# Kernel tuning notes

Measured on AMD Instinct MI355X. Metric: run time of the kernel, lower is better.

## Reference

```python
import jax, jax.numpy as jnp
import numpy as np

N, E = 50000, 200000
SIZES = [16, 32, 16]
EDIM = 8
EPS = 1e-5


def setup_inputs() -> dict:
    key = jax.random.key(0)
    ks = jax.random.split(key, 16)
    inp = {
        "x": jax.random.normal(ks[0], (N, SIZES[0]), jnp.float32),
        "edge_attr": jax.random.normal(ks[1], (E, EDIM), jnp.float32),
        "edge_index": jax.random.randint(ks[2], (2, E), 0, N, dtype=jnp.int32),
    }
    ki = 3
    for l in range(2):
        fin, fout = SIZES[l], SIZES[l + 1]
        m = fin * fout
        # xavier-ish init matching torch.nn.init.xavier_uniform_ scales
        inp[f"W1_{l}"] = jax.random.normal(ks[ki], (EDIM, m), jnp.float32) / np.float32(np.sqrt(EDIM)); ki += 1
        inp[f"b1_{l}"] = jnp.zeros((m,), jnp.float32)
        inp[f"W2_{l}"] = jax.random.normal(ks[ki], (m, m), jnp.float32) * np.float32(0.01 / np.sqrt(m)); ki += 1
        inp[f"b2_{l}"] = jnp.zeros((m,), jnp.float32)
        inp[f"root_{l}"] = jax.random.normal(ks[ki], (fin, fout), jnp.float32) / np.float32(np.sqrt(fin)); ki += 1
        inp[f"bias_{l}"] = jnp.zeros((fout,), jnp.float32)
        inp[f"gamma_{l}"] = jnp.ones((fout,), jnp.float32)
        inp[f"beta_{l}"] = jnp.zeros((fout,), jnp.float32)
    return inp


def _lrelu(v):
    return jnp.where(v >= 0, v, 0.01 * v)


def _nnconv(x, src, dst, edge_attr, W1, b1, W2, b2, root, bias, fin, fout):
    # edge MLP -> per-edge weight matrix [E, fin, fout]
    h = _lrelu(edge_attr @ W1 + b1) @ W2 + b2
    h = h.reshape(-1, fin, fout)
    # gather source node features, tiny per-edge matmul
    msg = jnp.einsum('ei,eio->eo', x[src], h)  # [E, fout]
    # scatter-mean aggregate at destination nodes
    agg = jax.ops.segment_sum(msg, dst, num_segments=N)
    deg = jax.ops.segment_sum(jnp.ones((msg.shape[0],), msg.dtype), dst, num_segments=N)
    agg = agg / jnp.maximum(deg, 1.0)[:, None]
    return agg + x @ root + bias


def _bn(v, gamma, beta):
    # BatchNorm1d (training mode: batch stats, biased variance)
    mu = v.mean(0)
    var = v.var(0)
    return (v - mu) * jax.lax.rsqrt(var + EPS) * gamma + beta


def reference(x, edge_attr,
              W1_0, b1_0, W2_0, b2_0, root_0, bias_0, gamma_0, beta_0,
              W1_1, b1_1, W2_1, b2_1, root_1, bias_1, gamma_1, beta_1,
              edge_index):
    src, dst = edge_index[0], edge_index[1]
    h = _nnconv(x, src, dst, edge_attr, W1_0, b1_0, W2_0, b2_0, root_0, bias_0, SIZES[0], SIZES[1])
    h = _lrelu(_bn(h, gamma_0, beta_0))
    h = _nnconv(h, src, dst, edge_attr, W1_1, b1_1, W2_1, b2_1, root_1, bias_1, SIZES[1], SIZES[2])
    return _bn(h, gamma_1, beta_1)
```

## Files before the change

### kernel.cpp

```cpp
#include <hip/hip_runtime.h>
#include <hip/hip_bf16.h>

typedef __attribute__((ext_vector_type(4))) float f32x4;
typedef __attribute__((ext_vector_type(8))) short s16x8;
typedef __attribute__((ext_vector_type(4))) int int4v;

#define DEVI __device__ __forceinline__

constexpr int NN = 50000;
constexpr int NE = 200000;
constexpr float BN_EPS = 1e-5f;

DEVI float bfbits2f(unsigned v) { union { unsigned u; float f; } t; t.u = v << 16; return t.f; }
DEVI float lrelu_f(float v) { return v >= 0.f ? v : 0.01f * v; }

__global__ void k_transpose_w2(const float* __restrict__ A0, const float* __restrict__ A1,
                               __hip_bfloat16* __restrict__ T0, __hip_bfloat16* __restrict__ T1) {
  const float* W2 = blockIdx.y ? A1 : A0;
  __hip_bfloat16* W2T = blockIdx.y ? T1 : T0;
  __shared__ float tile[32][33];
  int bx = blockIdx.x % 16, by = blockIdx.x / 16;
  int t = threadIdx.x;
  int r = t / 32, c = t % 32;
  for (int rr = r; rr < 32; rr += 8)
    tile[rr][c] = W2[(size_t)(by * 32 + rr) * 512 + bx * 32 + c];
  __syncthreads();
  for (int rr = r; rr < 32; rr += 8)
    W2T[(size_t)(bx * 32 + rr) * 512 + by * 32 + c] = __float2bfloat16(tile[c][rr]);
}

__global__ void k_transpose_w1(const float* __restrict__ A0, const float* __restrict__ A1,
                               __hip_bfloat16* __restrict__ T0, __hip_bfloat16* __restrict__ T1) {
  const float* W1 = blockIdx.y ? A1 : A0;
  __hip_bfloat16* W1T = blockIdx.y ? T1 : T0;
  int tid = blockIdx.x * 256 + threadIdx.x;
  if (tid < 8 * 512) {
    int k = tid / 512, n = tid % 512;
    W1T[n * 8 + k] = __float2bfloat16(W1[tid]);
  }
}

__global__ void k_count(const int* __restrict__ dst, int* __restrict__ cnt) {
  int e = blockIdx.x * 256 + threadIdx.x;
  if (e < NE) atomicAdd(&cnt[dst[e]], 1);
}

constexpr int SCAN_ELEMS = 1024;
__global__ void k_scan1(const int* __restrict__ cnt, int* __restrict__ base, int* __restrict__ aux, int n) {
  __shared__ int sw[256];
  int b = blockIdx.x, t = threadIdx.x;
  int i0 = b * SCAN_ELEMS + t * 4;
  int v[4]; int s = 0;
  #pragma unroll
  for (int j = 0; j < 4; j++) { int idx = i0 + j; v[j] = (idx < n) ? cnt[idx] : 0; s += v[j]; }
  sw[t] = s; __syncthreads();
  for (int d = 1; d < 256; d <<= 1) {
    int val = (t >= d) ? sw[t - d] : 0;
    __syncthreads();
    sw[t] += val;
    __syncthreads();
  }
  int run = (t > 0) ? sw[t - 1] : 0;
  #pragma unroll
  for (int j = 0; j < 4; j++) { int idx = i0 + j; if (idx < n) base[idx] = run; run += v[j]; }
  if (t == 255) aux[b] = sw[255];
}

__global__ void k_scan2(int* aux, int nb) {
  if (threadIdx.x == 0 && blockIdx.x == 0) {
    int run = 0;
    for (int i = 0; i < nb; i++) { int v = aux[i]; aux[i] = run; run += v; }
  }
}

__global__ void k_scan3(int* __restrict__ base, int* __restrict__ cursor, const int* __restrict__ aux, int n) {
  int i = blockIdx.x * 256 + threadIdx.x;
  if (i < n) { int v = base[i] + aux[i / SCAN_ELEMS]; base[i] = v; cursor[i] = v; }
}

__global__ void k_place(const int* __restrict__ dst, int* __restrict__ cursor, int* __restrict__ perm) {
  int e = blockIdx.x * 256 + threadIdx.x;
  if (e < NE) { int p = atomicAdd(&cursor[dst[e]], 1); perm[p] = e; }
}

template <int FIN, int FOUT>
__global__ __launch_bounds__(512, 2)
void k_edge(const float* __restrict__ x, const float* __restrict__ ea,
            const int* __restrict__ srcI,
            const __hip_bfloat16* __restrict__ W1T, const float* __restrict__ b1,
            const __hip_bfloat16* __restrict__ W2T, const float* __restrict__ b2,
            __hip_bfloat16* __restrict__ msgb)
{
  static_assert(FOUT == 32 || FOUT == 16, "");
  constexpr int TM = 512;
  constexpr int CG = 32;
  constexpr int NCGI = 16;
  constexpr int KH = 256;
  constexpr int NKC = 4;
  constexpr int NOT = FOUT / 16;
  constexpr int BSTRIDE = KH * 2 + 16;
  constexpr int XLDS = TM + 8;

  __shared__ __align__(16) char ubuf[65536];
  __shared__ __align__(16) __hip_bfloat16 eab[TM][8];
  __shared__ __align__(16) __hip_bfloat16 xlt[FIN][XLDS];

  const int tid = threadIdx.x;
  const int lane = tid & 63, w = tid >> 6;
  const int l15 = lane & 15, l4 = lane >> 4;
  const int e0 = blockIdx.x * TM;
  const int rem = min(TM, NE - e0);
  const int wrow0 = w * 64;

  {
    int er = e0 + min(tid, rem - 1);
    float4 v0 = *(const float4*)(ea + (size_t)er * 8);
    float4 v1 = *(const float4*)(ea + (size_t)er * 8 + 4);
    __hip_bfloat16* p = &eab[tid][0];
    p[0] = __float2bfloat16(v0.x); p[1] = __float2bfloat16(v0.y);
    p[2] = __float2bfloat16(v0.z); p[3] = __float2bfloat16(v0.w);
    p[4] = __float2bfloat16(v1.x); p[5] = __float2bfloat16(v1.y);
    p[6] = __float2bfloat16(v1.z); p[7] = __float2bfloat16(v1.w);
    int s = srcI[er];
    #pragma unroll
    for (int q = 0; q < FIN / 4; q++) {
      float4 xv4 = *(const float4*)(x + (size_t)s * FIN + q * 4);
      xlt[q * 4 + 0][tid] = __float2bfloat16(xv4.x);
      xlt[q * 4 + 1][tid] = __float2bfloat16(xv4.y);
      xlt[q * 4 + 2][tid] = __float2bfloat16(xv4.z);
      xlt[q * 4 + 3][tid] = __float2bfloat16(xv4.w);
    }
  }
  __syncthreads();

  f32x4 msg[4][NOT];
  #pragma unroll
  for (int rt = 0; rt < 4; rt++)
    #pragma unroll
    for (int ot = 0; ot < NOT; ot++) msg[rt][ot] = (f32x4)(0.f);

  s16x8 af[NKC][4][2];
  int4v sr0, sr1;

  for (int sw = 0; sw < 2; ++sw) {
    {
      int n = tid >> 4, s0 = tid & 15;
      const char* gp = (const char*)(W2T + (size_t)n * 512 + sw * KH);
      sr0 = *(const int4v*)(gp + s0 * 16);
      sr1 = *(const int4v*)(gp + (s0 + 16) * 16);
    }
    s16x8 afe[4];
    #pragma unroll
    for (int rt = 0; rt < 4; rt++) {
      s16x8 tv = *(const s16x8*)(&eab[wrow0 + rt * 16 + l15][0]);
      afe[rt] = (lane < 16) ? tv : (s16x8)0;
    }
    char* gme = ubuf + w * 8192;
    #pragma unroll
    for (int kc = 0; kc < NKC; kc++) {
      #pragma unroll
      for (int ct = 0; ct < 4; ct++) {
        int c = sw * KH + kc * 64 + ct * 16 + l15;
        s16x8 bw = *(const s16x8*)(W1T + c * 8);
        bw = (lane < 16) ? bw : (s16x8)0;
        float b1v = b1[c];
        #pragma unroll
        for (int rt = 0; rt < 4; rt++) {
          f32x4 d = __builtin_amdgcn_mfma_f32_16x16x32_bf16(afe[rt], bw, (f32x4)(0.f), 0, 0, 0);
          #pragma unroll
          for (int r = 0; r < 4; r++) {
            int rloc = rt * 16 + l4 * 4 + r;
            float gv = d[r] + b1v;
            gv = gv >= 0.f ? gv : 0.01f * gv;
            int byt = (rloc * 128 + (ct * 16 + l15) * 2) ^ (((rloc + (rloc >> 2)) & 3) << 5);
            *(__hip_bfloat16*)(gme + byt) = __float2bfloat16(gv);
          }
        }
      }
      #pragma unroll
      for (int rt = 0; rt < 4; rt++)
        #pragma unroll
        for (int ks = 0; ks < 2; ks++) {
          int rloc = rt * 16 + l15;
          int byt = (rloc * 128 + (ks * 32 + l4 * 8) * 2) ^ (((rloc + (rloc >> 2)) & 3) << 5);
          af[kc][rt][ks] = *(const s16x8*)(gme + byt);
        }
    }
    #pragma unroll
    for (int kc = 0; kc < NKC; kc++)
      #pragma unroll
      for (int rt = 0; rt < 4; rt++)
        #pragma unroll
        for (int ks = 0; ks < 2; ks++)
          asm volatile("" : "+v"(af[kc][rt][ks]));
    __syncthreads();
    {
      int n = tid >> 4, s0 = tid & 15;
      char* bb = ubuf;
      *(int4v*)(bb + n * BSTRIDE + s0 * 16) = sr0;
      *(int4v*)(bb + n * BSTRIDE + (s0 + 16) * 16) = sr1;
    }
    __syncthreads();

    for (int cgi = 0; cgi < NCGI; ++cgi) {
      if (cgi + 1 < NCGI) {
        int n = tid >> 4, s0 = tid & 15;
        const char* gp = (const char*)(W2T + (size_t)((cgi + 1) * CG + n) * 512 + sw * KH);
        sr0 = *(const int4v*)(gp + s0 * 16);
        sr1 = *(const int4v*)(gp + (s0 + 16) * 16);
      }
      const char* bb = ubuf + (cgi & 1) * (CG * BSTRIDE);
      f32x4 acc[4][2];
      #pragma unroll
      for (int rt = 0; rt < 4; rt++) { acc[rt][0] = (f32x4)(0.f); acc[rt][1] = (f32x4)(0.f); }

      #pragma unroll
      for (int kc = 0; kc < NKC; kc++)
        #pragma unroll
        for (int ct = 0; ct < 2; ct++) {
          int c = ct * 16 + l15;
          #pragma unroll
          for (int ks = 0; ks < 2; ks++) {
            const s16x8 bw = *(const s16x8*)(bb + c * BSTRIDE + kc * 128 + ks * 64 + l4 * 16);
            #pragma unroll
            for (int rt = 0; rt < 4; rt++)
              acc[rt][ct] = __builtin_amdgcn_mfma_f32_16x16x32_bf16(af[kc][rt][ks], bw, acc[rt][ct], 0, 0, 0);
          }
        }

      #pragma unroll
      for (int ct = 0; ct < 2; ct++) {
        float b2v = (sw == 0) ? b2[cgi * CG + ct * 16 + l15] : 0.f;
        const int iv = (FOUT == 32) ? cgi : (cgi * 2 + ct);
        const int ot = (FOUT == 32) ? ct : 0;
        #pragma unroll
        for (int rt = 0; rt < 4; rt++) {
          int rbase = wrow0 + rt * 16 + l4 * 4;
          ushort4 xv = *(const ushort4*)(&xlt[iv][rbase]);
          msg[rt][ot][0] += bfbits2f(xv.x) * (acc[rt][ct][0] + b2v);
          msg[rt][ot][1] += bfbits2f(xv.y) * (acc[rt][ct][1] + b2v);
          msg[rt][ot][2] += bfbits2f(xv.z) * (acc[rt][ct][2] + b2v);
          msg[rt][ot][3] += bfbits2f(xv.w) * (acc[rt][ct][3] + b2v);
        }
      }
      if (cgi + 1 < NCGI) {
        int n = tid >> 4, s0 = tid & 15;
        char* bw2 = ubuf + ((cgi + 1) & 1) * (CG * BSTRIDE);
        *(int4v*)(bw2 + n * BSTRIDE + s0 * 16) = sr0;
        *(int4v*)(bw2 + n * BSTRIDE + (s0 + 16) * 16) = sr1;
      }
      __syncthreads();
    }
  }

  #pragma unroll
  for (int rt = 0; rt < 4; rt++)
    #pragma unroll
    for (int r = 0; r < 4; r++) {
      int row = wrow0 + rt * 16 + l4 * 4 + r;
      if (row < rem) {
        #pragma unroll
        for (int ot = 0; ot < NOT; ot++)
          msgb[(size_t)(e0 + row) * FOUT + ot * 16 + l15] = __float2bfloat16(msg[rt][ot][r]);
      }
    }
}

template <int FIN, int FOUT>
__global__ void k_node_agg(const __hip_bfloat16* __restrict__ msgb, const int* __restrict__ perm,
                           const int* __restrict__ base,
                           const float* __restrict__ x,
                           const float* __restrict__ root,
                           const float* __restrict__ bias,
                           float* __restrict__ h)
{
  __shared__ float rl[FIN * FOUT];
  constexpr int NPB = 256 / FOUT;
  int t = threadIdx.x;
  for (int i = t; i < FIN * FOUT; i += 256) rl[i] = root[i];
  __syncthreads();
  int n = blockIdx.x * NPB + t / FOUT;
  int o = t % FOUT;
  if (n >= NN) return;
  int s = base[n];
  int e = (n + 1 < NN) ? base[n + 1] : NE;
  float sum = 0.f;
  for (int j = s; j < e; j++)
    sum += __bfloat162float(msgb[(size_t)perm[j] * FOUT + o]);
  float acc = sum / fmaxf((float)(e - s), 1.f) + bias[o];
  #pragma unroll
  for (int i = 0; i < FIN; i++)
    acc += x[(size_t)n * FIN + i] * rl[i * FOUT + o];
  h[(size_t)n * FOUT + o] = acc;
}

template <int FOUT>
__global__ void k_stats(const float* __restrict__ h, float* __restrict__ ssum, float* __restrict__ ssq) {
  constexpr int RPB = 256 / FOUT;
  int t = threadIdx.x;
  int o = t % FOUT, rr = t / FOUT;
  float v = 0.f, v2 = 0.f;
  for (int r = blockIdx.x * RPB + rr; r < NN; r += gridDim.x * RPB) {
    float y = h[(size_t)r * FOUT + o];
    v += y; v2 += y * y;
  }
  #pragma unroll
  for (int d = FOUT; d < 64; d <<= 1) { v += __shfl_xor(v, d); v2 += __shfl_xor(v2, d); }
  __shared__ float sv[4][32], sq[4][32];
  int wv = t >> 6, ln = t & 63;
  if (ln < FOUT) { sv[wv][ln] = v; sq[wv][ln] = v2; }
  __syncthreads();
  if (t < FOUT) {
    float a = 0.f, b = 0.f;
    #pragma unroll
    for (int w2 = 0; w2 < 4; w2++) { a += sv[w2][t]; b += sq[w2][t]; }
    atomicAdd(&ssum[t], a);
    atomicAdd(&ssq[t], b);
  }
}

template <int FOUT, bool LRELU>
__global__ void k_bn(const float* __restrict__ h, const float* __restrict__ ssum,
                     const float* __restrict__ ssq, const float* __restrict__ gamma,
                     const float* __restrict__ beta, float* __restrict__ out)
{
  int idx = blockIdx.x * 256 + threadIdx.x;
  if (idx * 4 >= NN * FOUT) return;
  float4 v = *(const float4*)(h + (size_t)idx * 4);
  float r[4] = {v.x, v.y, v.z, v.w};
  #pragma unroll
  for (int j = 0; j < 4; j++) {
    int o = (idx * 4 + j) % FOUT;
    float mu = ssum[o] * (1.f / NN);
    float var = ssq[o] * (1.f / NN) - mu * mu;
    float sc = rsqrtf(var + BN_EPS) * gamma[o];
    float y = (r[j] - mu) * sc + beta[o];
    if (LRELU) y = lrelu_f(y);
    r[j] = y;
  }
  *(float4*)(out + (size_t)idx * 4) = make_float4(r[0], r[1], r[2], r[3]);
}

extern "C" void kernel_launch(void* const* d_in, const int* in_sizes, int n_in,
                              void* d_out, int out_size, void* d_ws, size_t ws_size,
                              hipStream_t stream)
{
  const float* x0    = (const float*)d_in[0];
  const float* ea    = (const float*)d_in[1];
  const int*   ei    = (const int*)d_in[2];
  const float* W1_0  = (const float*)d_in[3];
  const float* b1_0  = (const float*)d_in[4];
  const float* W2_0  = (const float*)d_in[5];
  const float* b2_0  = (const float*)d_in[6];
  const float* root0 = (const float*)d_in[7];
  const float* bias0 = (const float*)d_in[8];
  const float* gam0  = (const float*)d_in[9];
  const float* bet0  = (const float*)d_in[10];
  const float* W1_1  = (const float*)d_in[11];
  const float* b1_1  = (const float*)d_in[12];
  const float* W2_1  = (const float*)d_in[13];
  const float* b2_1  = (const float*)d_in[14];
  const float* root1 = (const float*)d_in[15];
  const float* bias1 = (const float*)d_in[16];
  const float* gam1  = (const float*)d_in[17];
  const float* bet1  = (const float*)d_in[18];
  const int* srcI = ei;
  const int* dstI = ei + NE;

  char* ws = (char*)d_ws;
  size_t off = 0;
  auto alloc = [&](size_t bytes) { char* p = ws + off; off += (bytes + 255) & ~(size_t)255; return p; };
  int*   cnt   = (int*)alloc(50048 * 4);
  float* ssum0 = (float*)alloc(32 * 4);
  float* ssq0  = (float*)alloc(32 * 4);
  float* ssum1 = (float*)alloc(16 * 4);
  float* ssq1  = (float*)alloc(16 * 4);
  size_t zero_bytes = off;
  int*   base   = (int*)alloc(50048 * 4);
  int*   cursor = (int*)alloc(50048 * 4);
  int*   aux    = (int*)alloc(64 * 4);
  int*   perm   = (int*)alloc((size_t)NE * 4);
  __hip_bfloat16* msgb = (__hip_bfloat16*)alloc((size_t)NE * 32 * 2);
  float* h0 = (float*)alloc((size_t)NN * 32 * 4);
  float* h1 = (float*)alloc((size_t)NN * 16 * 4);
  float* x1 = (float*)alloc((size_t)NN * 32 * 4);
  __hip_bfloat16* W2T0 = (__hip_bfloat16*)alloc(512 * 512 * 2);
  __hip_bfloat16* W2T1 = (__hip_bfloat16*)alloc(512 * 512 * 2);
  __hip_bfloat16* W1T0 = (__hip_bfloat16*)alloc(512 * 8 * 2);
  __hip_bfloat16* W1T1 = (__hip_bfloat16*)alloc(512 * 8 * 2);

  hipMemsetAsync(d_ws, 0, zero_bytes, stream);

  k_transpose_w2<<<dim3(256, 2), 256, 0, stream>>>(W2_0, W2_1, W2T0, W2T1);
  k_transpose_w1<<<dim3(16, 2), 256, 0, stream>>>(W1_0, W1_1, W1T0, W1T1);

  constexpr int NSB = (NN + SCAN_ELEMS - 1) / SCAN_ELEMS;
  k_count<<<(NE + 255) / 256, 256, 0, stream>>>(dstI, cnt);
  k_scan1<<<NSB, 256, 0, stream>>>(cnt, base, aux, NN);
  k_scan2<<<1, 64, 0, stream>>>(aux, NSB);
  k_scan3<<<(NN + 255) / 256, 256, 0, stream>>>(base, cursor, aux, NN);
  k_place<<<(NE + 255) / 256, 256, 0, stream>>>(dstI, cursor, perm);

  constexpr int TM = 512;
  k_edge<16, 32><<<(NE + TM - 1) / TM, 512, 0, stream>>>(x0, ea, srcI, W1T0, b1_0, W2T0, b2_0, msgb);
  k_node_agg<16, 32><<<(NN + 7) / 8, 256, 0, stream>>>(msgb, perm, base, x0, root0, bias0, h0);
  k_stats<32><<<128, 256, 0, stream>>>(h0, ssum0, ssq0);
  k_bn<32, true><<<((NN * 32 / 4) + 255) / 256, 256, 0, stream>>>(h0, ssum0, ssq0, gam0, bet0, x1);

  k_edge<32, 16><<<(NE + TM - 1) / TM, 512, 0, stream>>>(x1, ea, srcI, W1T1, b1_1, W2T1, b2_1, msgb);
  k_node_agg<32, 16><<<(NN + 15) / 16, 256, 0, stream>>>(msgb, perm, base, x1, root1, bias1, h1);
  k_stats<16><<<128, 256, 0, stream>>>(h1, ssum1, ssq1);
  k_bn<16, false><<<((NN * 16 / 4) + 255) / 256, 256, 0, stream>>>(h1, ssum1, ssq1, gam1, bet1, (float*)d_out);
}
```

Baseline: 397.1 us.

## Use single-wave edge blocks and stream W2 fragments directly from global into registers

The edge kernel shrinks from 512-thread blocks of 512 edges to single-wavefront blocks of 64 edges. The cooperative LDS staging of W2 tiles and all the per-step block barriers are dropped. Each wave instead loads its MFMA B operands straight from global memory (L2/cache) with a two-stage register double buffer. This removes barrier and LDS traffic, but every wave now refetches the whole W2 matrix from cache, so L2 bandwidth demand rises sharply and global load latency may be exposed.

```diff
diff --git a/kernel.cpp b/kernel.cpp
--- a/kernel.cpp
+++ b/kernel.cpp
@@ -84,7 +84,7 @@
 }
 
 template <int FIN, int FOUT>
-__global__ __launch_bounds__(512, 2)
+__global__ __launch_bounds__(64, 2)
 void k_edge(const float* __restrict__ x, const float* __restrict__ ea,
             const int* __restrict__ srcI,
             const __hip_bfloat16* __restrict__ W1T, const float* __restrict__ b1,
@@ -92,31 +92,28 @@
             __hip_bfloat16* __restrict__ msgb)
 {
   static_assert(FOUT == 32 || FOUT == 16, "");
-  constexpr int TM = 512;
+  constexpr int TM = 64;
   constexpr int CG = 32;
   constexpr int NCGI = 16;
   constexpr int KH = 256;
   constexpr int NKC = 4;
   constexpr int NOT = FOUT / 16;
-  constexpr int BSTRIDE = KH * 2 + 16;
   constexpr int XLDS = TM + 8;
 
-  __shared__ __align__(16) char ubuf[65536];
+  __shared__ __align__(16) char gme[64 * 128];
   __shared__ __align__(16) __hip_bfloat16 eab[TM][8];
   __shared__ __align__(16) __hip_bfloat16 xlt[FIN][XLDS];
 
-  const int tid = threadIdx.x;
-  const int lane = tid & 63, w = tid >> 6;
+  const int lane = threadIdx.x & 63;
   const int l15 = lane & 15, l4 = lane >> 4;
   const int e0 = blockIdx.x * TM;
   const int rem = min(TM, NE - e0);
-  const int wrow0 = w * 64;
 
   {
-    int er = e0 + min(tid, rem - 1);
+    int er = e0 + min(lane, rem - 1);
     float4 v0 = *(const float4*)(ea + (size_t)er * 8);
     float4 v1 = *(const float4*)(ea + (size_t)er * 8 + 4);
-    __hip_bfloat16* p = &eab[tid][0];
+    __hip_bfloat16* p = &eab[lane][0];
     p[0] = __float2bfloat16(v0.x); p[1] = __float2bfloat16(v0.y);
     p[2] = __float2bfloat16(v0.z); p[3] = __float2bfloat16(v0.w);
     p[4] = __float2bfloat16(v1.x); p[5] = __float2bfloat16(v1.y);
@@ -125,10 +122,10 @@
     #pragma unroll
     for (int q = 0; q < FIN / 4; q++) {
       float4 xv4 = *(const float4*)(x + (size_t)s * FIN + q * 4);
-      xlt[q * 4 + 0][tid] = __float2bfloat16(xv4.x);
-      xlt[q * 4 + 1][tid] = __float2bfloat16(xv4.y);
-      xlt[q * 4 + 2][tid] = __float2bfloat16(xv4.z);
-      xlt[q * 4 + 3][tid] = __float2bfloat16(xv4.w);
+      xlt[q * 4 + 0][lane] = __float2bfloat16(xv4.x);
+      xlt[q * 4 + 1][lane] = __float2bfloat16(xv4.y);
+      xlt[q * 4 + 2][lane] = __float2bfloat16(xv4.z);
+      xlt[q * 4 + 3][lane] = __float2bfloat16(xv4.w);
     }
   }
   __syncthreads();
@@ -140,22 +137,15 @@
     for (int ot = 0; ot < NOT; ot++) msg[rt][ot] = (f32x4)(0.f);
 
   s16x8 af[NKC][4][2];
-  int4v sr0, sr1;
+  int4v bwreg[2][2];
 
   for (int sw = 0; sw < 2; ++sw) {
-    {
-      int n = tid >> 4, s0 = tid & 15;
-      const char* gp = (const char*)(W2T + (size_t)n * 512 + sw * KH);
-      sr0 = *(const int4v*)(gp + s0 * 16);
-      sr1 = *(const int4v*)(gp + (s0 + 16) * 16);
-    }
     s16x8 afe[4];
     #pragma unroll
     for (int rt = 0; rt < 4; rt++) {
-      s16x8 tv = *(const s16x8*)(&eab[wrow0 + rt * 16 + l15][0]);
+      s16x8 tv = *(const s16x8*)(&eab[rt * 16 + l15][0]);
       afe[rt] = (lane < 16) ? tv : (s16x8)0;
     }
-    char* gme = ubuf + w * 8192;
     #pragma unroll
     for (int kc = 0; kc < NKC; kc++) {
       #pragma unroll
@@ -193,40 +183,35 @@
         #pragma unroll
         for (int ks = 0; ks < 2; ks++)
           asm volatile("" : "+v"(af[kc][rt][ks]));
-    __syncthreads();
-    {
-      int n = tid >> 4, s0 = tid & 15;
-      char* bb = ubuf;
-      *(int4v*)(bb + n * BSTRIDE + s0 * 16) = sr0;
-      *(int4v*)(bb + n * BSTRIDE + (s0 + 16) * 16) = sr1;
-    }
-    __syncthreads();
-
+
+    const char* Wbase = (const char*)W2T + (size_t)sw * KH * 2;
+    auto loadB = [&](int cgi2, int stg, int4v* dst) {
+      const int ct = stg & 1, kc = stg >> 1;
+      #pragma unroll
+      for (int ks = 0; ks < 2; ks++) {
+        int col = cgi2 * CG + ct * 16 + l15;
+        int koff = kc * 64 + ks * 32 + l4 * 8;
+        dst[ks] = *(const int4v*)(Wbase + (size_t)col * 1024 + koff * 2);
+      }
+    };
+
+    loadB(0, 0, bwreg[0]);
     for (int cgi = 0; cgi < NCGI; ++cgi) {
-      if (cgi + 1 < NCGI) {
-        int n = tid >> 4, s0 = tid & 15;
-        const char* gp = (const char*)(W2T + (size_t)((cgi + 1) * CG + n) * 512 + sw * KH);
-        sr0 = *(const int4v*)(gp + s0 * 16);
-        sr1 = *(const int4v*)(gp + (s0 + 16) * 16);
-      }
-      const char* bb = ubuf + (cgi & 1) * (CG * BSTRIDE);
       f32x4 acc[4][2];
       #pragma unroll
       for (int rt = 0; rt < 4; rt++) { acc[rt][0] = (f32x4)(0.f); acc[rt][1] = (f32x4)(0.f); }
 
       #pragma unroll
-      for (int kc = 0; kc < NKC; kc++)
-        #pragma unroll
-        for (int ct = 0; ct < 2; ct++) {
-          int c = ct * 16 + l15;
+      for (int s = 0; s < 8; ++s) {
+        if (s < 7) loadB(cgi, s + 1, bwreg[(s + 1) & 1]);
+        else if (cgi + 1 < NCGI) loadB(cgi + 1, 0, bwreg[0]);
+        const int ct = s & 1, kc = s >> 1;
+        #pragma unroll
+        for (int ks = 0; ks < 2; ks++)
           #pragma unroll
-          for (int ks = 0; ks < 2; ks++) {
-            const s16x8 bw = *(const s16x8*)(bb + c * BSTRIDE + kc * 128 + ks * 64 + l4 * 16);
-            #pragma unroll
-            for (int rt = 0; rt < 4; rt++)
-              acc[rt][ct] = __builtin_amdgcn_mfma_f32_16x16x32_bf16(af[kc][rt][ks], bw, acc[rt][ct], 0, 0, 0);
-          }
-        }
+          for (int rt = 0; rt < 4; rt++)
+            acc[rt][ct] = __builtin_amdgcn_mfma_f32_16x16x32_bf16(af[kc][rt][ks], bwreg[s & 1][ks], acc[rt][ct], 0, 0, 0);
+      }
 
       #pragma unroll
       for (int ct = 0; ct < 2; ct++) {
@@ -235,7 +220,7 @@
         const int ot = (FOUT == 32) ? ct : 0;
         #pragma unroll
         for (int rt = 0; rt < 4; rt++) {
-          int rbase = wrow0 + rt * 16 + l4 * 4;
+          int rbase = rt * 16 + l4 * 4;
           ushort4 xv = *(const ushort4*)(&xlt[iv][rbase]);
           msg[rt][ot][0] += bfbits2f(xv.x) * (acc[rt][ct][0] + b2v);
           msg[rt][ot][1] += bfbits2f(xv.y) * (acc[rt][ct][1] + b2v);
@@ -243,13 +228,6 @@
           msg[rt][ot][3] += bfbits2f(xv.w) * (acc[rt][ct][3] + b2v);
         }
       }
-      if (cgi + 1 < NCGI) {
-        int n = tid >> 4, s0 = tid & 15;
-        char* bw2 = ubuf + ((cgi + 1) & 1) * (CG * BSTRIDE);
-        *(int4v*)(bw2 + n * BSTRIDE + s0 * 16) = sr0;
-        *(int4v*)(bw2 + n * BSTRIDE + (s0 + 16) * 16) = sr1;
-      }
-      __syncthreads();
     }
   }
 
@@ -257,7 +235,7 @@
   for (int rt = 0; rt < 4; rt++)
     #pragma unroll
     for (int r = 0; r < 4; r++) {
-      int row = wrow0 + rt * 16 + l4 * 4 + r;
+      int row = rt * 16 + l4 * 4 + r;
       if (row < rem) {
         #pragma unroll
         for (int ot = 0; ot < NOT; ot++)
@@ -401,13 +379,13 @@
   k_scan3<<<(NN + 255) / 256, 256, 0, stream>>>(base, cursor, aux, NN);
   k_place<<<(NE + 255) / 256, 256, 0, stream>>>(dstI, cursor, perm);
 
-  constexpr int TM = 512;
-  k_edge<16, 32><<<(NE + TM - 1) / TM, 512, 0, stream>>>(x0, ea, srcI, W1T0, b1_0, W2T0, b2_0, msgb);
+  constexpr int TM = 64;
+  k_edge<16, 32><<<(NE + TM - 1) / TM, 64, 0, stream>>>(x0, ea, srcI, W1T0, b1_0, W2T0, b2_0, msgb);
   k_node_agg<16, 32><<<(NN + 7) / 8, 256, 0, stream>>>(msgb, perm, base, x0, root0, bias0, h0);
   k_stats<32><<<128, 256, 0, stream>>>(h0, ssum0, ssq0);
   k_bn<32, true><<<((NN * 32 / 4) + 255) / 256, 256, 0, stream>>>(h0, ssum0, ssq0, gam0, bet0, x1);
 
-  k_edge<32, 16><<<(NE + TM - 1) / TM, 512, 0, stream>>>(x1, ea, srcI, W1T1, b1_1, W2T1, b2_1, msgb);
+  k_edge<32, 16><<<(NE + TM - 1) / TM, 64, 0, stream>>>(x1, ea, srcI, W1T1, b1_1, W2T1, b2_1, msgb);
   k_node_agg<32, 16><<<(NN + 15) / 16, 256, 0, stream>>>(msgb, perm, base, x1, root1, bias1, h1);
   k_stats<16><<<128, 256, 0, stream>>>(h1, ssum1, ssq1);
   k_bn<16, false><<<((NN * 16 / 4) + 255) / 256, 256, 0, stream>>>(h1, ssum1, ssq1, gam1, bet1, (float*)d_out);
```

Result: slower. 640.3 us (+61.2%).

## Shrink edge-kernel LDS by shuffling edge attributes and halving scratch

Applied to the files above, without the earlier changes.

Removes the shared-memory edge-attribute staging buffer and instead builds the MFMA A-fragments via cross-lane shuffles, dropping an initial block barrier. The per-wave first-layer scratch is halved by processing the four row tiles in two passes, and the shared buffer is sized to exactly the double-buffered W2 tile. The goal is to lower LDS footprint so more blocks can be resident per CU, at the cost of extra shuffles and a second pass over W1 fragment loads.

```diff
diff --git a/kernel.cpp b/kernel.cpp
--- a/kernel.cpp
+++ b/kernel.cpp
@@ -101,8 +101,7 @@
   constexpr int BSTRIDE = KH * 2 + 16;
   constexpr int XLDS = TM + 8;
 
-  __shared__ __align__(16) char ubuf[65536];
-  __shared__ __align__(16) __hip_bfloat16 eab[TM][8];
+  __shared__ __align__(16) char ubuf[2 * CG * BSTRIDE];
   __shared__ __align__(16) __hip_bfloat16 xlt[FIN][XLDS];
 
   const int tid = threadIdx.x;
@@ -112,15 +111,24 @@
   const int rem = min(TM, NE - e0);
   const int wrow0 = w * 64;
 
+  s16x8 afe[4];
   {
     int er = e0 + min(tid, rem - 1);
     float4 v0 = *(const float4*)(ea + (size_t)er * 8);
     float4 v1 = *(const float4*)(ea + (size_t)er * 8 + 4);
-    __hip_bfloat16* p = &eab[tid][0];
+    union { s16x8 v; int i4[4]; } earow;
+    __hip_bfloat16* p = (__hip_bfloat16*)&earow;
     p[0] = __float2bfloat16(v0.x); p[1] = __float2bfloat16(v0.y);
     p[2] = __float2bfloat16(v0.z); p[3] = __float2bfloat16(v0.w);
     p[4] = __float2bfloat16(v1.x); p[5] = __float2bfloat16(v1.y);
     p[6] = __float2bfloat16(v1.z); p[7] = __float2bfloat16(v1.w);
+    #pragma unroll
+    for (int rt = 0; rt < 4; rt++) {
+      union { s16x8 v; int i4[4]; } t2;
+      #pragma unroll
+      for (int q = 0; q < 4; q++) t2.i4[q] = __shfl(earow.i4[q], rt * 16 + l15);
+      afe[rt] = (lane < 16) ? t2.v : (s16x8)0;
+    }
     int s = srcI[er];
     #pragma unroll
     for (int q = 0; q < FIN / 4; q++) {
@@ -131,7 +139,6 @@
       xlt[q * 4 + 3][tid] = __float2bfloat16(xv4.w);
     }
   }
-  __syncthreads();
 
   f32x4 msg[4][NOT];
   #pragma unroll
@@ -149,42 +156,39 @@
       sr0 = *(const int4v*)(gp + s0 * 16);
       sr1 = *(const int4v*)(gp + (s0 + 16) * 16);
     }
-    s16x8 afe[4];
-    #pragma unroll
-    for (int rt = 0; rt < 4; rt++) {
-      s16x8 tv = *(const s16x8*)(&eab[wrow0 + rt * 16 + l15][0]);
-      afe[rt] = (lane < 16) ? tv : (s16x8)0;
-    }
-    char* gme = ubuf + w * 8192;
-    #pragma unroll
-    for (int kc = 0; kc < NKC; kc++) {
-      #pragma unroll
-      for (int ct = 0; ct < 4; ct++) {
-        int c = sw * KH + kc * 64 + ct * 16 + l15;
-        s16x8 bw = *(const s16x8*)(W1T + c * 8);
-        bw = (lane < 16) ? bw : (s16x8)0;
-        float b1v = b1[c];
-        #pragma unroll
-        for (int rt = 0; rt < 4; rt++) {
-          f32x4 d = __builtin_amdgcn_mfma_f32_16x16x32_bf16(afe[rt], bw, (f32x4)(0.f), 0, 0, 0);
+    char* gme = ubuf + w * 4096;
+    #pragma unroll
+    for (int h = 0; h < 2; ++h) {
+      #pragma unroll
+      for (int kc = 0; kc < NKC; kc++) {
+        #pragma unroll
+        for (int ct = 0; ct < 4; ct++) {
+          int c = sw * KH + kc * 64 + ct * 16 + l15;
+          s16x8 bw = *(const s16x8*)(W1T + c * 8);
+          bw = (lane < 16) ? bw : (s16x8)0;
+          float b1v = b1[c];
           #pragma unroll
-          for (int r = 0; r < 4; r++) {
-            int rloc = rt * 16 + l4 * 4 + r;
-            float gv = d[r] + b1v;
-            gv = gv >= 0.f ? gv : 0.01f * gv;
-            int byt = (rloc * 128 + (ct * 16 + l15) * 2) ^ (((rloc + (rloc >> 2)) & 3) << 5);
-            *(__hip_bfloat16*)(gme + byt) = __float2bfloat16(gv);
+          for (int rt2 = 0; rt2 < 2; rt2++) {
+            f32x4 d = __builtin_amdgcn_mfma_f32_16x16x32_bf16(afe[h * 2 + rt2], bw, (f32x4)(0.f), 0, 0, 0);
+            #pragma unroll
+            for (int r = 0; r < 4; r++) {
+              int rloc = rt2 * 16 + l4 * 4 + r;
+              float gv = d[r] + b1v;
+              gv = gv >= 0.f ? gv : 0.01f * gv;
+              int byt = (rloc * 128 + (ct * 16 + l15) * 2) ^ (((rloc + (rloc >> 2)) & 3) << 5);
+              *(__hip_bfloat16*)(gme + byt) = __float2bfloat16(gv);
+            }
           }
         }
+        #pragma unroll
+        for (int rt2 = 0; rt2 < 2; rt2++)
+          #pragma unroll
+          for (int ks = 0; ks < 2; ks++) {
+            int rloc = rt2 * 16 + l15;
+            int byt = (rloc * 128 + (ks * 32 + l4 * 8) * 2) ^ (((rloc + (rloc >> 2)) & 3) << 5);
+            af[kc][h * 2 + rt2][ks] = *(const s16x8*)(gme + byt);
+          }
       }
-      #pragma unroll
-      for (int rt = 0; rt < 4; rt++)
-        #pragma unroll
-        for (int ks = 0; ks < 2; ks++) {
-          int rloc = rt * 16 + l15;
-          int byt = (rloc * 128 + (ks * 32 + l4 * 8) * 2) ^ (((rloc + (rloc >> 2)) & 3) << 5);
-          af[kc][rt][ks] = *(const s16x8*)(gme + byt);
-        }
     }
     #pragma unroll
     for (int kc = 0; kc < NKC; kc++)
@@ -196,9 +200,8 @@
     __syncthreads();
     {
       int n = tid >> 4, s0 = tid & 15;
-      char* bb = ubuf;
-      *(int4v*)(bb + n * BSTRIDE + s0 * 16) = sr0;
-      *(int4v*)(bb + n * BSTRIDE + (s0 + 16) * 16) = sr1;
+      *(int4v*)(ubuf + n * BSTRIDE + s0 * 16) = sr0;
+      *(int4v*)(ubuf + n * BSTRIDE + (s0 + 16) * 16) = sr1;
     }
     __syncthreads();
 
```

After: 389.6 us. Within noise of the previous version (-1.9%).
